# Kernel tuning notes

Hardware: AMD Instinct MI355X
Metric: run time of the kernel (lower is better)

The kernel has to match this reference:

```python
import jax, jax.numpy as jnp
import numpy as np

N_NODES = 50000
N_EDGES = 800000
IN_C = 16
HID_C = 16
OUT_C = 10
N_GRAPHS = 500
EDGE_DIM = 3
MLP_HID = 25
BN_EPS = 1e-5


def setup_inputs() -> dict:
    key = jax.random.key(0)
    ks = iter(jax.random.split(key, 40))

    def nrm(shape, scale=1.0):
        return jax.random.normal(next(ks), shape, dtype=jnp.float32) * scale

    inp = {}
    inp["x"] = nrm((N_NODES, IN_C))
    inp["edge_index"] = jax.random.randint(next(ks), (2, N_EDGES), 0, N_NODES, dtype=jnp.int32)
    inp["edge_attr"] = jax.random.uniform(next(ks), (N_EDGES, EDGE_DIM), dtype=jnp.float32)
    inp["batch"] = jnp.sort(jax.random.randint(next(ks), (N_NODES,), 0, N_GRAPHS, dtype=jnp.int32))

    def bn_params():
        g = jax.random.uniform(next(ks), (MLP_HID,), minval=0.8, maxval=1.2, dtype=jnp.float32)
        b = nrm((MLP_HID,), 0.1)
        mu = nrm((MLP_HID,), 0.1)
        var = jax.random.uniform(next(ks), (MLP_HID,), minval=0.5, maxval=1.5, dtype=jnp.float32)
        return g, b, mu, var

    # edge MLP 1: 3 -> 25 -> IN_C*HID_C
    inp["W1a"] = nrm((EDGE_DIM, MLP_HID), 0.3)
    inp["b1a"] = nrm((MLP_HID,), 0.05)
    inp["g1"], inp["bt1"], inp["m1"], inp["v1"] = bn_params()
    inp["W1b"] = nrm((MLP_HID, IN_C * HID_C), 0.1)
    inp["b1b"] = nrm((IN_C * HID_C,), 0.05)
    inp["root1"] = nrm((IN_C, HID_C), 0.2)
    inp["bias1"] = nrm((HID_C,), 0.05)

    # edge MLP 2: 3 -> 25 -> HID_C*HID_C
    inp["W2a"] = nrm((EDGE_DIM, MLP_HID), 0.3)
    inp["b2a"] = nrm((MLP_HID,), 0.05)
    inp["g2"], inp["bt2"], inp["m2"], inp["v2"] = bn_params()
    inp["W2b"] = nrm((MLP_HID, HID_C * HID_C), 0.1)
    inp["b2b"] = nrm((HID_C * HID_C,), 0.05)
    inp["root2"] = nrm((HID_C, HID_C), 0.2)
    inp["bias2"] = nrm((HID_C,), 0.05)

    # final MLP([HID_C, OUT_C]) -> single plain linear (plain_last)
    inp["fcW"] = nrm((HID_C, OUT_C), 0.2)
    inp["fcb"] = nrm((OUT_C,), 0.05)
    return inp


def _edge_mlp(e, Wa, ba, g, bt, mu, var, Wb, bb):
    # Linear -> BatchNorm(eval) -> ReLU -> (dropout=eval identity) -> Linear
    h = e @ Wa + ba
    h = g * (h - mu) * jax.lax.rsqrt(var + BN_EPS) + bt
    h = jax.nn.relu(h)
    return h @ Wb + bb


def _nnconv(x, src, dst, w_edge, root, bias, out_dim):
    # message: x_j [E,in] times per-edge weight [E,in,out]
    msg = jnp.einsum("ei,eio->eo", x[src], w_edge)
    agg = jax.ops.segment_sum(msg, dst, num_segments=N_NODES)
    deg = jax.ops.segment_sum(jnp.ones((src.shape[0],), msg.dtype), dst, num_segments=N_NODES)
    agg = agg / jnp.maximum(deg, 1.0)[:, None]  # mean aggregation
    return agg + x @ root + bias


def reference(x, edge_index, edge_attr, batch,
              W1a, b1a, g1, bt1, m1, v1, W1b, b1b, root1, bias1,
              W2a, b2a, g2, bt2, m2, v2, W2b, b2b, root2, bias2,
              fcW, fcb):
    src, dst = edge_index[0], edge_index[1]

    w1 = _edge_mlp(edge_attr, W1a, b1a, g1, bt1, m1, v1, W1b, b1b).reshape(-1, IN_C, HID_C)
    x = jax.nn.elu(_nnconv(x, src, dst, w1, root1, bias1, HID_C))

    w2 = _edge_mlp(edge_attr, W2a, b2a, g2, bt2, m2, v2, W2b, b2b).reshape(-1, HID_C, HID_C)
    x = jax.nn.elu(_nnconv(x, src, dst, w2, root2, bias2, HID_C))

    # global mean pooling over graphs
    pooled = jax.ops.segment_sum(x, batch, num_segments=N_GRAPHS)
    cnt = jax.ops.segment_sum(jnp.ones((x.shape[0],), x.dtype), batch, num_segments=N_GRAPHS)
    pooled = pooled / jnp.maximum(cnt, 1.0)[:, None]

    return pooled @ fcW + fcb  # [N_GRAPHS, OUT_C]
```

## Files before the change

### kernel.cpp

```cpp
#include <hip/hip_runtime.h>
#include <math.h>

#define N_NODES 50000
#define N_EDGES 800000
#define IN_C 16
#define HID_C 16
#define OUT_C 10
#define N_GRAPHS 500
#define EDGE_DIM 3
#define MLP_HID 25
#define BN_EPS 1e-5f

#define SCAN_NB ((N_NODES + 255) / 256)
#define NZB 200

typedef __attribute__((ext_vector_type(8))) _Float16 half8;
typedef __attribute__((ext_vector_type(2))) _Float16 half2v;
typedef __attribute__((ext_vector_type(4))) float f32x4;
union U4H8 { uint4 u; half8 h; half2v p[4]; };
union HU { _Float16 h; unsigned short u; };


__global__ __launch_bounds__(256) void setup_kernel(
    const float* __restrict__ W1a, const float* __restrict__ b1a,
    const float* __restrict__ g1, const float* __restrict__ bt1,
    const float* __restrict__ m1, const float* __restrict__ v1,
    const float* __restrict__ W2a, const float* __restrict__ b2a,
    const float* __restrict__ g2, const float* __restrict__ bt2,
    const float* __restrict__ m2, const float* __restrict__ v2,
    const float* __restrict__ W1b, const float* __restrict__ b1b,
    const float* __restrict__ W2b, const float* __restrict__ b2b,
    const int* __restrict__ batch,
    const float* __restrict__ xin, const float* __restrict__ eattr,
    float* __restrict__ AC1, float* __restrict__ AC2,
    unsigned int* __restrict__ WF1, unsigned int* __restrict__ WF2,
    int* __restrict__ goff, int* __restrict__ cnt,
    float4* __restrict__ ea4, unsigned int* __restrict__ xh0,
    int* __restrict__ ticket)
{
    const int blk = blockIdx.x;
    const int tid = threadIdx.x;
    if (blk < 7) {
        int t = blk * 256 + tid;
        if (t >= 1664) return;
        const float *Wb, *bb; unsigned int *WH;
        int tl = t;
        if (t < 832) { Wb = W1b; bb = b1b; WH = WF1; }
        else { tl = t - 832; Wb = W2b; bb = b2b; WH = WF2; }
        int m = tl >> 6;
        int L = tl & 63;
        int q = L >> 4, o = L & 15;
        unsigned int hi[8];
        for (int j = 0; j < 8; ++j) {
            int kp = m*32 + q*8 + j;
            int k = kp >> 4, i = kp & 15;
            float w = (k < 25) ? Wb[k*256 + i*16 + o] : bb[i*16 + o];
            HU cv; cv.h = (_Float16)w;
            hi[j] = cv.u;
        }
        int base = (m*64 + L) * 4;
        for (int d = 0; d < 4; ++d)
            WH[base + d] = hi[2*d] | (hi[2*d+1] << 16);
        return;
    }
    if (blk == 7 || blk == 8) {
        if (blk == 7) {
            if (tid < 26) {
                int k = tid;
                if (k < 25) {
                    float sc = g1[k] / sqrtf(v1[k] + BN_EPS);
                    AC1[k*4+0] = sc * W1a[0*MLP_HID+k];
                    AC1[k*4+1] = sc * W1a[1*MLP_HID+k];
                    AC1[k*4+2] = sc * W1a[2*MLP_HID+k];
                    AC1[k*4+3] = sc * (b1a[k] - m1[k]) + bt1[k];
                } else {
                    AC1[100] = 0.f; AC1[101] = 0.f; AC1[102] = 0.f; AC1[103] = 1.f;
                }
            } else if (tid >= 32 && tid < 58) {
                int k = tid - 32;
                if (k < 25) {
                    float sc = g2[k] / sqrtf(v2[k] + BN_EPS);
                    AC2[k*4+0] = sc * W2a[0*MLP_HID+k];
                    AC2[k*4+1] = sc * W2a[1*MLP_HID+k];
                    AC2[k*4+2] = sc * W2a[2*MLP_HID+k];
                    AC2[k*4+3] = sc * (b2a[k] - m2[k]) + bt2[k];
                } else {
                    AC2[100] = 0.f; AC2[101] = 0.f; AC2[102] = 0.f; AC2[103] = 1.f;
                }
            }
        }
        int g = (blk - 7) * 256 + tid;
        if (g <= N_GRAPHS) {
            int lo = 0, hi = N_NODES;
            while (lo < hi) {
                int mid = (lo + hi) >> 1;
                if (batch[mid] < g) lo = mid + 1; else hi = mid;
            }
            goff[g] = lo;
        }
        return;
    }
    const int bt = (blk - 9) * 256 + tid;
    const int STR = NZB * 256;
    int4* c4 = (int4*)cnt;
    const int4 z4 = {0, 0, 0, 0};
    for (int i = bt; i < 12500; i += STR) c4[i] = z4;
    for (int e = bt; e < N_EDGES; e += STR) {
        float4 a;
        a.x = eattr[e*3+0];
        a.y = eattr[e*3+1];
        a.z = eattr[e*3+2];
        a.w = 0.f;
        ea4[e] = a;
    }
    const float2* x2 = (const float2*)xin;
    for (int i = bt; i < 400000; i += STR) {
        float2 v = x2[i];
        HU h0; h0.h = (_Float16)v.x;
        HU h1; h1.h = (_Float16)v.y;
        xh0[i] = (unsigned int)h0.u | ((unsigned int)h1.u << 16);
    }
    if (blk == 9 && tid == 0) *ticket = 0;
}


__global__ __launch_bounds__(256) void rank_kernel(const int* __restrict__ dst,
                                                   int* __restrict__ cnt,
                                                   int* __restrict__ rank) {
    int e = blockIdx.x * blockDim.x + threadIdx.x;
    if (e < N_EDGES) rank[e] = atomicAdd(&cnt[dst[e]], 1);
}

__global__ __launch_bounds__(256) void scan_p1(const int* __restrict__ cnt,
                                               int* __restrict__ bsum,
                                               int* __restrict__ bpre,
                                               int* __restrict__ off,
                                               int* __restrict__ ticket) {
    __shared__ int lds[256];
    __shared__ int sDone;
    int t = threadIdx.x;
    int idx = blockIdx.x * 256 + t;
    lds[t] = (idx < N_NODES) ? cnt[idx] : 0;
    __syncthreads();
    for (int d = 128; d > 0; d >>= 1) {
        if (t < d) lds[t] += lds[t + d];
        __syncthreads();
    }
    if (t == 0) {
        bsum[blockIdx.x] = lds[0];
        __threadfence();
        sDone = atomicAdd(ticket, 1);
    }
    __syncthreads();
    if (sDone != SCAN_NB - 1) return;
    __threadfence();
    int v = (t < SCAN_NB) ? bsum[t] : 0;
    __syncthreads();
    lds[t] = v;
    __syncthreads();
    for (int d = 1; d < 256; d <<= 1) {
        int u = (t >= d) ? lds[t - d] : 0;
        __syncthreads();
        lds[t] += u;
        __syncthreads();
    }
    if (t < SCAN_NB) bpre[t] = (t > 0) ? lds[t - 1] : 0;
    if (t == 255) off[N_NODES] = lds[255];
}

__global__ __launch_bounds__(256) void scan_p3(const int* __restrict__ cnt,
                                               const int* __restrict__ bpre,
                                               int* __restrict__ off) {
    __shared__ int lds[256];
    int t = threadIdx.x;
    int idx = blockIdx.x * 256 + t;
    int v = (idx < N_NODES) ? cnt[idx] : 0;
    lds[t] = v;
    __syncthreads();
    for (int d = 1; d < 256; d <<= 1) {
        int u = (t >= d) ? lds[t - d] : 0;
        __syncthreads();
        lds[t] += u;
        __syncthreads();
    }
    if (idx < N_NODES) off[idx] = bpre[blockIdx.x] + lds[t] - v;
}


__global__ __launch_bounds__(256) void edge_mfma7_kernel(
    const unsigned short* __restrict__ xh,
    const int* __restrict__ src,
    const int* __restrict__ dst,
    const int* __restrict__ rank,
    const int* __restrict__ off,
    const float4* __restrict__ ea4,
    const float* __restrict__ AC,
    const unsigned int* __restrict__ WF,
    float* __restrict__ msg_buf)
{
    __shared__ uint4 wf_s[832];
    const int tid = threadIdx.x;
    #pragma unroll
    for (int it = 0; it < 4; ++it) {
        int gi = tid + it*256;
        if (gi < 832) wf_s[gi] = ((const uint4*)WF)[gi];
    }
    __syncthreads();

    const int wave = tid >> 6;
    const int lane = tid & 63;
    const int q    = lane >> 4;
    const int el   = lane & 15;
    const int i0   = (q & 1) * 8;
    const bool bsel = (q >> 1) != 0;
    const int E0   = (blockIdx.x * 4 + wave) * 64;

    const int sAll = src[E0 + lane];
    const int dAll = dst[E0 + lane];
    const int rAll = rank[E0 + lane];
    const int pAll = off[dAll] + rAll;

    int   sT[4];
    float a0[4], a1[4], a2[4];
    #pragma unroll
    for (int t = 0; t < 4; ++t) {
        sT[t] = __shfl(sAll, t*16 + el);
        float4 at = ea4[E0 + t*16 + el];
        a0[t] = at.x; a1[t] = at.y; a2[t] = at.z;
    }

    U4H8 xf[4];
    #pragma unroll
    for (int t = 0; t < 4; ++t)
        xf[t].u = *(const uint4*)(const void*)(xh + (size_t)sT[t]*16 + i0);

    f32x4 acc0 = {0.f,0.f,0.f,0.f}, acc1 = {0.f,0.f,0.f,0.f};
    f32x4 acc2 = {0.f,0.f,0.f,0.f}, acc3 = {0.f,0.f,0.f,0.f};
    #pragma unroll 1
    for (int m = 0; m < 13; ++m) {
        const float4 Ae = *(const float4*)(AC + m*8);
        const float4 Ao = *(const float4*)(AC + m*8 + 4);
        const float A0 = bsel ? Ao.x : Ae.x;
        const float A1 = bsel ? Ao.y : Ae.y;
        const float A2 = bsel ? Ao.z : Ae.z;
        const float A3 = bsel ? Ao.w : Ae.w;
        U4H8 w; w.u = wf_s[m*64 + lane];
        #pragma unroll
        for (int t = 0; t < 4; ++t) {
            float h = fmaxf(fmaf(a2[t], A2, fmaf(a1[t], A1,
                              fmaf(a0[t], A0, A3))), 0.f);
            _Float16 hh = (_Float16)h;
            half2v h2; h2.x = hh; h2.y = hh;
            U4H8 f;
            #pragma unroll
            for (int j = 0; j < 4; ++j) f.p[j] = h2 * xf[t].p[j];
            f32x4 a = (t==0) ? acc0 : (t==1) ? acc1 : (t==2) ? acc2 : acc3;
            a = __builtin_amdgcn_mfma_f32_16x16x32_f16(w.h, f.h, a, 0, 0, 0);
            if (t==0) acc0 = a; else if (t==1) acc1 = a;
            else if (t==2) acc2 = a; else acc3 = a;
        }
    }

    #pragma unroll
    for (int t = 0; t < 4; ++t) {
        int row = __shfl(pAll, t*16 + el);
        f32x4 a = (t==0) ? acc0 : (t==1) ? acc1 : (t==2) ? acc2 : acc3;
        *(f32x4*)(msg_buf + (size_t)row * HID_C + q*4) = a;
    }
}

__global__ __launch_bounds__(256) void node_gather_kernel(
    const float* __restrict__ xin, const float* __restrict__ msg_buf,
    const int* __restrict__ off,
    const float* __restrict__ root, const float* __restrict__ bias,
    float* __restrict__ xout, unsigned int* __restrict__ xh_out)
{
    __shared__ float root_s[IN_C * HID_C];
    if (threadIdx.x < 64)
        ((float4*)root_s)[threadIdx.x] = ((const float4*)root)[threadIdx.x];
    __syncthreads();

    int t = blockIdx.x * blockDim.x + threadIdx.x;
    int n = t >> 2;
    if (n >= N_NODES) return;
    int c0 = (t & 3) * 4;
    int lo = off[n], hi = off[n+1];
    float inv = 1.f / fmaxf((float)(hi - lo), 1.f);

    const f32x4* m4 = (const f32x4*)msg_buf;
    const int qi = c0 >> 2;
    f32x4 s0 = {0.f,0.f,0.f,0.f}, s1 = {0.f,0.f,0.f,0.f};
    int r = lo;
    for (; r + 2 <= hi; r += 2) {
        s0 += m4[(size_t)r*4 + qi];
        s1 += m4[(size_t)(r+1)*4 + qi];
    }
    if (r < hi) s0 += m4[(size_t)r*4 + qi];
    f32x4 s = s0 + s1;

    const float4 bv = *(const float4*)(bias + c0);
    f32x4 acc;
    acc.x = fmaf(s.x, inv, bv.x);
    acc.y = fmaf(s.y, inv, bv.y);
    acc.z = fmaf(s.z, inv, bv.z);
    acc.w = fmaf(s.w, inv, bv.w);

    const float4* x4 = (const float4*)(xin + (size_t)n * IN_C);
    #pragma unroll
    for (int j = 0; j < 4; ++j) {
        float4 xv = x4[j];
        #pragma unroll
        for (int k = 0; k < 4; ++k) {
            float xi = (k==0) ? xv.x : (k==1) ? xv.y : (k==2) ? xv.z : xv.w;
            const float4 rv = *(const float4*)(root_s + (j*4+k)*HID_C + c0);
            acc.x = fmaf(xi, rv.x, acc.x);
            acc.y = fmaf(xi, rv.y, acc.y);
            acc.z = fmaf(xi, rv.z, acc.z);
            acc.w = fmaf(xi, rv.w, acc.w);
        }
    }

    acc.x = acc.x > 0.f ? acc.x : (expf(acc.x) - 1.f);
    acc.y = acc.y > 0.f ? acc.y : (expf(acc.y) - 1.f);
    acc.z = acc.z > 0.f ? acc.z : (expf(acc.z) - 1.f);
    acc.w = acc.w > 0.f ? acc.w : (expf(acc.w) - 1.f);
    *(f32x4*)(xout + (size_t)n * HID_C + c0) = acc;

    if (xh_out) {
        HU h0, h1, h2, h3;
        h0.h = (_Float16)acc.x; h1.h = (_Float16)acc.y;
        h2.h = (_Float16)acc.z; h3.h = (_Float16)acc.w;
        uint2 pk;
        pk.x = (unsigned int)h0.u | ((unsigned int)h1.u << 16);
        pk.y = (unsigned int)h2.u | ((unsigned int)h3.u << 16);
        ((uint2*)xh_out)[n*4 + qi] = pk;
    }
}

__global__ __launch_bounds__(64) void pool_final_kernel(
    const float* __restrict__ xin, const int* __restrict__ goff,
    const float* __restrict__ fcW, const float* __restrict__ fcb,
    float* __restrict__ out)
{
    __shared__ float part[4][HID_C];
    __shared__ float pooled[HID_C];
    int g = blockIdx.x;
    int t = threadIdx.x;
    int c = t & 15, sub = t >> 4;
    int lo = goff[g], hi = goff[g+1];
    float s = 0.f;
    for (int n = lo + sub; n < hi; n += 4)
        s += xin[(size_t)n*HID_C + c];
    part[sub][c] = s;
    __syncthreads();
    if (t < HID_C) {
        pooled[t] = (part[0][t] + part[1][t] + part[2][t] + part[3][t])
                    / fmaxf((float)(hi - lo), 1.f);
    }
    __syncthreads();
    if (t < OUT_C) {
        float acc = fcb[t];
        #pragma unroll
        for (int i = 0; i < HID_C; ++i)
            acc = fmaf(pooled[i], fcW[i*OUT_C+t], acc);
        out[g*OUT_C + t] = acc;
    }
}


extern "C" void kernel_launch(void* const* d_in, const int* in_sizes, int n_in,
                              void* d_out, int out_size, void* d_ws, size_t ws_size,
                              hipStream_t stream)
{
    const float* x     = (const float*)d_in[0];
    const int*   ei    = (const int*)d_in[1];
    const float* eattr = (const float*)d_in[2];
    const int*   batch = (const int*)d_in[3];
    const float* W1a   = (const float*)d_in[4];
    const float* b1a   = (const float*)d_in[5];
    const float* g1    = (const float*)d_in[6];
    const float* bt1   = (const float*)d_in[7];
    const float* m1    = (const float*)d_in[8];
    const float* v1    = (const float*)d_in[9];
    const float* W1b   = (const float*)d_in[10];
    const float* b1b   = (const float*)d_in[11];
    const float* root1 = (const float*)d_in[12];
    const float* bias1 = (const float*)d_in[13];
    const float* W2a   = (const float*)d_in[14];
    const float* b2a   = (const float*)d_in[15];
    const float* g2    = (const float*)d_in[16];
    const float* bt2   = (const float*)d_in[17];
    const float* m2    = (const float*)d_in[18];
    const float* v2    = (const float*)d_in[19];
    const float* W2b   = (const float*)d_in[20];
    const float* b2b   = (const float*)d_in[21];
    const float* root2 = (const float*)d_in[22];
    const float* bias2 = (const float*)d_in[23];
    const float* fcW   = (const float*)d_in[24];
    const float* fcb   = (const float*)d_in[25];

    const int* src = ei;
    const int* dst = ei + N_EDGES;

    float* ws   = (float*)d_ws;
    float* MSG  = ws;
    float* X1   = ws + 12800000;
    float* X2   = ws + 13600000;
    int*   RANK = (int*)(ws + 14400000);
    int*   CNT  = (int*)(ws + 15200000);
    int*   OFF  = (int*)(ws + 15250000);
    int*   GOFF = (int*)(ws + 15300064);
    unsigned int* WF1 = (unsigned int*)(ws + 15300576);
    unsigned int* WF2 = (unsigned int*)(ws + 15303904);
    float* AC1  = ws + 15307232;
    float* AC2  = ws + 15307344;
    int*   BSUM = (int*)(ws + 15307456);
    int*   BPRE = (int*)(ws + 15307712);
    int*   TICK = (int*)(ws + 15307968);
    float* EA4  = ws + 15308032;
    unsigned int* XH0 = (unsigned int*)(ws + 18508032);
    unsigned int* XH1 = (unsigned int*)(ws + 18908032);

    setup_kernel<<<9 + NZB, 256, 0, stream>>>(
        W1a, b1a, g1, bt1, m1, v1, W2a, b2a, g2, bt2, m2, v2,
        W1b, b1b, W2b, b2b, batch, x, eattr,
        AC1, AC2, WF1, WF2, GOFF, CNT, (float4*)EA4, XH0, TICK);
    rank_kernel<<<N_EDGES/256, 256, 0, stream>>>(dst, CNT, RANK);
    scan_p1<<<SCAN_NB, 256, 0, stream>>>(CNT, BSUM, BPRE, OFF, TICK);
    scan_p3<<<SCAN_NB, 256, 0, stream>>>(CNT, BPRE, OFF);

    edge_mfma7_kernel<<<N_EDGES/256, 256, 0, stream>>>(
        (const unsigned short*)XH0, src, dst, RANK, OFF,
        (const float4*)EA4, AC1, WF1, MSG);
    node_gather_kernel<<<(N_NODES*4 + 255)/256, 256, 0, stream>>>(
        x, MSG, OFF, root1, bias1, X1, XH1);

    edge_mfma7_kernel<<<N_EDGES/256, 256, 0, stream>>>(
        (const unsigned short*)XH1, src, dst, RANK, OFF,
        (const float4*)EA4, AC2, WF2, MSG);
    node_gather_kernel<<<(N_NODES*4 + 255)/256, 256, 0, stream>>>(
        X1, MSG, OFF, root2, bias2, X2, (unsigned int*)nullptr);

    pool_final_kernel<<<N_GRAPHS, 64, 0, stream>>>(X2, GOFF, fcW, fcb, (float*)d_out);
}
```

Before: 251.4 us.

## Fold rank atomics into setup and merge two-pass scan into one kernel

Moves the per-edge atomic rank counting into the setup kernel's grid-stride loop and drops the separate rank kernel. The two scan kernels become one: the last block to finish scans the block sums and publishes a release flag, and the other blocks spin on that flag before writing offsets. Count, ticket and flag are cleared with a single memset, so there are fewer kernel launches and inter-kernel gaps. In exchange, the edge atomics now run over only 200 blocks, and the spin-wait relies on all scan blocks being resident at once.

```diff
diff --git a/kernel.cpp b/kernel.cpp
--- a/kernel.cpp
+++ b/kernel.cpp
@@ -19,7 +19,6 @@
 typedef __attribute__((ext_vector_type(4))) float f32x4;
 union U4H8 { uint4 u; half8 h; half2v p[4]; };
 union HU { _Float16 h; unsigned short u; };
-
 
 __global__ __launch_bounds__(256) void setup_kernel(
     const float* __restrict__ W1a, const float* __restrict__ b1a,
@@ -32,11 +31,11 @@
     const float* __restrict__ W2b, const float* __restrict__ b2b,
     const int* __restrict__ batch,
     const float* __restrict__ xin, const float* __restrict__ eattr,
+    const int* __restrict__ dst,
     float* __restrict__ AC1, float* __restrict__ AC2,
     unsigned int* __restrict__ WF1, unsigned int* __restrict__ WF2,
-    int* __restrict__ goff, int* __restrict__ cnt,
-    float4* __restrict__ ea4, unsigned int* __restrict__ xh0,
-    int* __restrict__ ticket)
+    int* __restrict__ goff, int* __restrict__ cnt, int* __restrict__ rank_out,
+    float4* __restrict__ ea4, unsigned int* __restrict__ xh0)
 {
     const int blk = blockIdx.x;
     const int tid = threadIdx.x;
@@ -102,9 +101,6 @@
     }
     const int bt = (blk - 9) * 256 + tid;
     const int STR = NZB * 256;
-    int4* c4 = (int4*)cnt;
-    const int4 z4 = {0, 0, 0, 0};
-    for (int i = bt; i < 12500; i += STR) c4[i] = z4;
     for (int e = bt; e < N_EDGES; e += STR) {
         float4 a;
         a.x = eattr[e*3+0];
@@ -120,42 +116,20 @@
         HU h1; h1.h = (_Float16)v.y;
         xh0[i] = (unsigned int)h0.u | ((unsigned int)h1.u << 16);
     }
-    if (blk == 9 && tid == 0) *ticket = 0;
-}
-
-
-__global__ __launch_bounds__(256) void rank_kernel(const int* __restrict__ dst,
-                                                   int* __restrict__ cnt,
-                                                   int* __restrict__ rank) {
-    int e = blockIdx.x * blockDim.x + threadIdx.x;
-    if (e < N_EDGES) rank[e] = atomicAdd(&cnt[dst[e]], 1);
-}
-
-__global__ __launch_bounds__(256) void scan_p1(const int* __restrict__ cnt,
-                                               int* __restrict__ bsum,
-                                               int* __restrict__ bpre,
-                                               int* __restrict__ off,
-                                               int* __restrict__ ticket) {
+    for (int e = bt; e < N_EDGES; e += STR)
+        rank_out[e] = atomicAdd(&cnt[dst[e]], 1);
+}
+
+__global__ __launch_bounds__(256) void scan_kernel(
+    const int* __restrict__ cnt, int* __restrict__ bsum,
+    int* __restrict__ bpre, int* __restrict__ off,
+    int* __restrict__ ticket, int* __restrict__ flag)
+{
     __shared__ int lds[256];
     __shared__ int sDone;
     int t = threadIdx.x;
     int idx = blockIdx.x * 256 + t;
-    lds[t] = (idx < N_NODES) ? cnt[idx] : 0;
-    __syncthreads();
-    for (int d = 128; d > 0; d >>= 1) {
-        if (t < d) lds[t] += lds[t + d];
-        __syncthreads();
-    }
-    if (t == 0) {
-        bsum[blockIdx.x] = lds[0];
-        __threadfence();
-        sDone = atomicAdd(ticket, 1);
-    }
-    __syncthreads();
-    if (sDone != SCAN_NB - 1) return;
-    __threadfence();
-    int v = (t < SCAN_NB) ? bsum[t] : 0;
-    __syncthreads();
+    int v = (idx < N_NODES) ? cnt[idx] : 0;
     lds[t] = v;
     __syncthreads();
     for (int d = 1; d < 256; d <<= 1) {
@@ -164,28 +138,43 @@
         lds[t] += u;
         __syncthreads();
     }
-    if (t < SCAN_NB) bpre[t] = (t > 0) ? lds[t - 1] : 0;
-    if (t == 255) off[N_NODES] = lds[255];
-}
-
-__global__ __launch_bounds__(256) void scan_p3(const int* __restrict__ cnt,
-                                               const int* __restrict__ bpre,
-                                               int* __restrict__ off) {
-    __shared__ int lds[256];
-    int t = threadIdx.x;
-    int idx = blockIdx.x * 256 + t;
-    int v = (idx < N_NODES) ? cnt[idx] : 0;
-    lds[t] = v;
-    __syncthreads();
-    for (int d = 1; d < 256; d <<= 1) {
-        int u = (t >= d) ? lds[t - d] : 0;
+    const int myincl = lds[t];
+    const int btot   = lds[255];
+    if (t == 0) {
+        bsum[blockIdx.x] = btot;
+        __threadfence();
+        sDone = atomicAdd(ticket, 1);
+    }
+    __syncthreads();
+    if (sDone == SCAN_NB - 1) {
+        __threadfence();
+        int b = (t < SCAN_NB) ? bsum[t] : 0;
         __syncthreads();
-        lds[t] += u;
+        lds[t] = b;
         __syncthreads();
-    }
-    if (idx < N_NODES) off[idx] = bpre[blockIdx.x] + lds[t] - v;
-}
-
+        for (int d = 1; d < 256; d <<= 1) {
+            int u = (t >= d) ? lds[t - d] : 0;
+            __syncthreads();
+            lds[t] += u;
+            __syncthreads();
+        }
+        if (t < SCAN_NB) bpre[t] = (t > 0) ? lds[t - 1] : 0;
+        if (t == 255) off[N_NODES] = lds[255];
+        __threadfence();
+        if (t == 0)
+            __hip_atomic_store(flag, 1, __ATOMIC_RELEASE,
+                               __HIP_MEMORY_SCOPE_AGENT);
+    } else {
+        if (t == 0) {
+            while (__hip_atomic_load(flag, __ATOMIC_RELAXED,
+                                     __HIP_MEMORY_SCOPE_AGENT) == 0)
+                __builtin_amdgcn_s_sleep(2);
+            __threadfence();
+        }
+        __syncthreads();
+    }
+    if (idx < N_NODES) off[idx] = bpre[blockIdx.x] + myincl - v;
+}
 
 __global__ __launch_bounds__(256) void edge_mfma7_kernel(
     const unsigned short* __restrict__ xh,
@@ -408,7 +397,9 @@
     float* X2   = ws + 13600000;
     int*   RANK = (int*)(ws + 14400000);
     int*   CNT  = (int*)(ws + 15200000);
-    int*   OFF  = (int*)(ws + 15250000);
+    int*   TICK = (int*)(ws + 15250000);
+    int*   FLAG = (int*)(ws + 15250004/4*0 + 15250001);
+    int*   OFF  = (int*)(ws + 15250016);
     int*   GOFF = (int*)(ws + 15300064);
     unsigned int* WF1 = (unsigned int*)(ws + 15300576);
     unsigned int* WF2 = (unsigned int*)(ws + 15303904);
@@ -416,18 +407,17 @@
     float* AC2  = ws + 15307344;
     int*   BSUM = (int*)(ws + 15307456);
     int*   BPRE = (int*)(ws + 15307712);
-    int*   TICK = (int*)(ws + 15307968);
     float* EA4  = ws + 15308032;
     unsigned int* XH0 = (unsigned int*)(ws + 18508032);
     unsigned int* XH1 = (unsigned int*)(ws + 18908032);
 
+    hipMemsetAsync(CNT, 0, 50016 * sizeof(int), stream);
+
     setup_kernel<<<9 + NZB, 256, 0, stream>>>(
         W1a, b1a, g1, bt1, m1, v1, W2a, b2a, g2, bt2, m2, v2,
-        W1b, b1b, W2b, b2b, batch, x, eattr,
-        AC1, AC2, WF1, WF2, GOFF, CNT, (float4*)EA4, XH0, TICK);
-    rank_kernel<<<N_EDGES/256, 256, 0, stream>>>(dst, CNT, RANK);
-    scan_p1<<<SCAN_NB, 256, 0, stream>>>(CNT, BSUM, BPRE, OFF, TICK);
-    scan_p3<<<SCAN_NB, 256, 0, stream>>>(CNT, BPRE, OFF);
+        W1b, b1b, W2b, b2b, batch, x, eattr, dst,
+        AC1, AC2, WF1, WF2, GOFF, CNT, RANK, (float4*)EA4, XH0);
+    scan_kernel<<<SCAN_NB, 256, 0, stream>>>(CNT, BSUM, BPRE, OFF, TICK, FLAG);
 
     edge_mfma7_kernel<<<N_EDGES/256, 256, 0, stream>>>(
         (const unsigned short*)XH0, src, dst, RANK, OFF,
```

Result: slower. 261.2 us (+3.9%).
